# Performance work log

Measured on AMD Instinct MI355X. Metric: run time of the kernel, lower is better.

The kernel has to match this reference:

```python
import jax, jax.numpy as jnp
import numpy as np
from jax import lax

KEY_SIZE, WIDTH, CH = 4, 32, 3  # hardcoded in construct_mapping(4, 32, 3)


def _inv_perm():
    # Reproduce construct_mapping: mapping[0]=arange, mapping[1]=t (a permutation).
    # tensor_map does out[:, t[i]] = in[:, i]  ==>  out = in[:, argsort(t)].
    s = np.arange(KEY_SIZE * WIDTH * CH)
    x = s.reshape(KEY_SIZE, WIDTH, CH)
    blocks = [x[:, j:j + KEY_SIZE, :].reshape(-1) for j in range(0, WIDTH, KEY_SIZE)]
    t = np.stack(blocks, 0).reshape(-1)
    return np.argsort(t)

_INV = jnp.asarray(_inv_perm())  # [384]


def setup_inputs() -> dict:
    key = jax.random.key(0)
    ks = jax.random.split(key, 8)
    B = 8192
    return {
        "x": jax.random.normal(ks[0], (B, 32, 32, 3), jnp.float32),
        "W": jax.random.normal(ks[1], (48, 48), jnp.float32) / np.float32(np.sqrt(48.0)),
        "conv1_w": jax.random.normal(ks[2], (10, 3, 5, 5), jnp.float32) * 0.1,
        "conv1_b": jnp.zeros((10,), jnp.float32),
        "conv2_w": jax.random.normal(ks[3], (20, 10, 5, 5), jnp.float32) * 0.05,
        "conv2_b": jnp.zeros((20,), jnp.float32),
        "fc1_w": jax.random.normal(ks[4], (50, 500), jnp.float32) * 0.04,
        "fc1_b": jnp.zeros((50,), jnp.float32),
        "fc2_w": jax.random.normal(ks[5], (10, 50), jnp.float32) * 0.1,
        "fc2_b": jnp.zeros((10,), jnp.float32),
    }


def _conv(x, w, b):
    y = lax.conv_general_dilated(x, w, (1, 1), 'VALID',
                                 dimension_numbers=('NCHW', 'OIHW', 'NCHW'))
    return y + b[None, :, None, None]


def _maxpool2(x):
    return lax.reduce_window(x, -jnp.inf, lax.max, (1, 1, 2, 2), (1, 1, 2, 2), 'VALID')


def reference(x, W, conv1_w, conv1_b, conv2_w, conv2_b, fc1_w, fc1_b, fc2_w, fc2_b):
    B = x.shape[0]
    # 4x4x3 blocks in row-major block order (i outer, j inner): [B, 64, 48]
    xb = x.reshape(B, 8, 4, 8, 4, 3).transpose(0, 1, 3, 2, 4, 5).reshape(B, 64, 48)
    y = jnp.einsum('bnk,jk->bnj', xb, W)          # per-block Linear (no bias), batched GEMM
    y = y.reshape(B, 8, 384)[:, :, _INV]          # per-row permutation (fused gather)
    img = y.reshape(B, 32, 32, 3).transpose(0, 3, 1, 2)  # NHWC -> NCHW
    h = jax.nn.relu(_maxpool2(_conv(img, conv1_w, conv1_b)))       # [B,10,14,14]
    h = jax.nn.relu(_maxpool2(_conv(h, conv2_w, conv2_b)))         # dropout2d: eval = identity; [B,20,5,5]
    h = h.reshape(-1, 500)
    h = jax.nn.relu(h @ fc1_w.T + fc1_b)          # dropout: eval = identity
    logits = h @ fc2_w.T + fc2_b
    return jax.nn.log_softmax(logits, axis=-1)
```

## Files before the change

kernel.cpp:

```cpp
#include <hip/hip_runtime.h>
#include <math.h>


typedef __attribute__((ext_vector_type(8))) short bf16x8;
typedef __attribute__((ext_vector_type(4))) float f32x4;

union Frag { short4 h[2]; bf16x8 v; };

static __device__ __forceinline__ unsigned short f2bf(float f) {
    union { float f; unsigned u; } v; v.f = f;
    unsigned r = v.u + 0x7FFFu + ((v.u >> 16) & 1u);
    return (unsigned short)(r >> 16);
}

#define MFMA(a, b, c) __builtin_amdgcn_mfma_f32_16x16x32_bf16((a), (b), (c), 0, 0, 0)

__global__ __launch_bounds__(64)
void prepack(const float* __restrict__ W, const float* __restrict__ w1,
             const float* __restrict__ w2, unsigned short* __restrict__ ws) {
    const int fid = blockIdx.x;
    const int lane = threadIdx.x;
    const int col = lane & 15, grp = lane >> 4;
    unsigned short tmp[8];
    #pragma unroll
    for (int e = 0; e < 8; ++e) {
        const int kap = 16 * (e >> 2) + 4 * grp + (e & 3);
        float v = 0.f;
        if (fid < 6) {
            const int ks = fid / 3, nt = fid % 3;
            const int k = 32 * ks + kap, j = 16 * nt + col;
            if (k < 48) v = W[j * 48 + k];
        } else if (fid < 11) {
            const int ky = fid - 6;
            const int kx = kap >> 2, icp = kap & 3;
            if (kx < 5 && icp < 3 && col < 10)
                v = w1[col * 75 + icp * 25 + ky * 5 + kx];
        } else {
            const int r = fid - 11, nt = r / 10, ky = (r % 10) >> 1, s = r & 1;
            const int idx = 32 * s + kap;
            const int kx = idx / 12, icp = idx % 12, oc = 16 * nt + col;
            if (kx < 5 && icp < 10 && oc < 20)
                v = w2[oc * 250 + icp * 25 + ky * 5 + kx];
        }
        tmp[e] = f2bf(v);
    }
    Frag f;
    f.h[0] = make_short4((short)tmp[0], (short)tmp[1], (short)tmp[2], (short)tmp[3]);
    f.h[1] = make_short4((short)tmp[4], (short)tmp[5], (short)tmp[6], (short)tmp[7]);
    *(bf16x8*)(ws + fid * 512 + lane * 8) = f.v;
}

__global__ __launch_bounds__(256)
void pack_fc1(const float* __restrict__ fw1, unsigned short* __restrict__ ws) {
    const int i = blockIdx.x * 256 + threadIdx.x;
    if (i < 12500) {
        const unsigned lo = f2bf(fw1[2 * i]);
        const unsigned hi = f2bf(fw1[2 * i + 1]);
        ((unsigned*)(ws + 16384))[i] = lo | (hi << 16);
    }
}

#define RS1 160
#define IMG_SZ 5184
#define RS2 168
#define H1_SZ 2416
#define AUXF 848

__global__ __launch_bounds__(512)
void fused_net(const float* __restrict__ x,
               const unsigned short* __restrict__ ws,
               const float* __restrict__ b1,
               const float* __restrict__ b2,
               const float* __restrict__ fb1,
               const float* __restrict__ fw2,
               const float* __restrict__ fb2,
               float* __restrict__ out)
{
    const int tid  = threadIdx.x;
    const int wave = __builtin_amdgcn_readfirstlane(tid >> 6);
    const int img  = wave >> 2;
    const int wv   = wave & 3;
    const int lane = tid & 63;
    const int col16 = lane & 15, grp = lane >> 4;

    __shared__ __align__(16) unsigned short s_pool[2 * IMG_SZ];
    __shared__ __align__(16) unsigned short s_h1[2 * H1_SZ];
    __shared__ __align__(16) float s_aux[2 * AUXF];

    unsigned short* s_img = s_pool + img * IMG_SZ;
    unsigned short* s_h1i = s_h1 + img * H1_SZ;
    unsigned short* s_b2  = s_pool;
    float* aux    = s_aux + img * AUXF;
    float* s_h2   = aux;

    const size_t bb = (size_t)(2 * blockIdx.x + img);

    {
        const int blkA = 16 * wv + col16;
        const float* xb = x + bb * 3072 + (blkA >> 3) * 384 + (blkA & 7) * 12;
        const int k0 = 4 * grp,      o0 = (k0 / 12) * 96 + (k0 % 12);
        const int k1 = 16 + 4 * grp, o1 = (k1 / 12) * 96 + (k1 % 12);
        const int k2 = 32 + 4 * grp, o2 = (k2 / 12) * 96 + (k2 % 12);
        const float4 fa = *(const float4*)(xb + o0);
        const float4 fb = *(const float4*)(xb + o1);
        const float4 fc = *(const float4*)(xb + o2);
        Frag a0, a1;
        a0.h[0] = make_short4((short)f2bf(fa.x), (short)f2bf(fa.y), (short)f2bf(fa.z), (short)f2bf(fa.w));
        a0.h[1] = make_short4((short)f2bf(fb.x), (short)f2bf(fb.y), (short)f2bf(fb.z), (short)f2bf(fb.w));
        a1.h[0] = make_short4((short)f2bf(fc.x), (short)f2bf(fc.y), (short)f2bf(fc.z), (short)f2bf(fc.w));
        a1.h[1] = make_short4(0, 0, 0, 0);

        #pragma unroll
        for (int nt = 0; nt < 3; ++nt) {
            Frag bl0, bl1;
            bl0.v = *(const bf16x8*)(ws + nt * 512 + lane * 8);
            bl1.v = *(const bf16x8*)(ws + (3 + nt) * 512 + lane * 8);
            f32x4 acc = {0.f, 0.f, 0.f, 0.f};
            acc = MFMA(a0.v, bl0.v, acc);
            acc = MFMA(a1.v, bl1.v, acc);
            const int j = 16 * nt + col16;
            const int di = j / 12, dj = (j % 12) / 3, cch = j % 3;
            #pragma unroll
            for (int r = 0; r < 4; ++r) {
                const int blk = 16 * wv + 4 * grp + r;
                const int row = (blk >> 3) * 4 + di, cp = (blk & 7) * 4 + dj;
                s_img[row * RS1 + cp * 4 + cch] = f2bf(acc[r]);
            }
        }
    }
    for (int p = tid; p < 2048; p += 512) {
        unsigned short* si = s_pool + (p >> 10) * IMG_SZ;
        const int q = p & 1023;
        si[(q >> 5) * RS1 + (q & 31) * 4 + 3] = 0;
    }
    for (int p = tid; p < 2048; p += 512) {
        unsigned short* si = s_pool + (p >> 10) * IMG_SZ;
        const int q = p & 1023;
        si[(q >> 5) * RS1 + 128 + (q & 31)] = 0;
    }
    if (tid < 128) s_pool[(tid >> 6) * IMG_SZ + 32 * RS1 + (tid & 63)] = 0;
    if (tid < 128) s_h1[(tid >> 6) * H1_SZ + 14 * RS2 + (tid & 63)] = 0;
    __syncthreads();

    {
        Frag bc1[5];
        #pragma unroll
        for (int f = 0; f < 5; ++f)
            bc1[f].v = *(const bf16x8*)(ws + (6 + f) * 512 + lane * 8);
        const float bias1 = b1[col16 < 10 ? col16 : 0];

        for (int t = wv; t < 49; t += 4) {
            const int q = 4 * t + (col16 >> 2), sub = col16 & 3;
            const int oi = q / 14, oj = q % 14;
            const int ci = 2 * oi + (sub >> 1), cj = 2 * oj + (sub & 1);
            const int base = ci * RS1 + cj * 4 + 4 * grp;
            f32x4 acc = {0.f, 0.f, 0.f, 0.f};
            #pragma unroll
            for (int ky = 0; ky < 5; ++ky) {
                Frag a;
                a.h[0] = *(const short4*)&s_img[base + ky * RS1];
                a.h[1] = *(const short4*)&s_img[base + ky * RS1 + 16];
                acc = MFMA(a.v, bc1[ky].v, acc);
            }
            const int qo = 4 * t + grp;
            if (col16 < 12) {
                const float pm = fmaxf(fmaxf(acc[0], acc[1]), fmaxf(acc[2], acc[3]));
                const float val = fmaxf(pm + bias1, 0.f);
                s_h1i[(qo / 14) * RS2 + (qo % 14) * 12 + col16] =
                    (col16 < 10) ? f2bf(val) : (unsigned short)0;
            }
        }
    }
    __syncthreads();

    {
        const uint4* src = (const uint4*)(ws + 11 * 512);
        uint4* dst = (uint4*)s_pool;
        dst[tid]       = src[tid];
        dst[tid + 512] = src[tid + 512];
        if (tid < 256) dst[tid + 1024] = src[tid + 1024];
    }
    __syncthreads();

    {
        const int oc1 = 16 + col16;
        const float bias20 = b2[col16];
        const float bias21 = b2[oc1 < 20 ? oc1 : 0];

        int baseA[2];
        #pragma unroll
        for (int tt = 0; tt < 2; ++tt) {
            const int t = wv + 4 * tt;
            int q = 4 * t + (col16 >> 2); if (q > 24) q = 24;
            const int sub = col16 & 3;
            const int oi = q / 5, oj = q % 5;
            const int ci = 2 * oi + (sub >> 1), cj = 2 * oj + (sub & 1);
            baseA[tt] = ci * RS2 + cj * 12 + 4 * grp;
        }

        f32x4 accA0 = {0.f,0.f,0.f,0.f}, accA1 = {0.f,0.f,0.f,0.f};
        f32x4 accB0 = {0.f,0.f,0.f,0.f}, accB1 = {0.f,0.f,0.f,0.f};
        #pragma unroll
        for (int ky = 0; ky < 5; ++ky) {
            #pragma unroll
            for (int s = 0; s < 2; ++s) {
                Frag bb0, bb1;
                bb0.v = *(const bf16x8*)(s_b2 + (ky * 2 + s) * 512 + lane * 8);
                bb1.v = *(const bf16x8*)(s_b2 + (10 + ky * 2 + s) * 512 + lane * 8);
                Frag a0, a1;
                a0.h[0] = *(const short4*)&s_h1i[baseA[0] + ky * RS2 + 32 * s];
                a0.h[1] = *(const short4*)&s_h1i[baseA[0] + ky * RS2 + 32 * s + 16];
                a1.h[0] = *(const short4*)&s_h1i[baseA[1] + ky * RS2 + 32 * s];
                a1.h[1] = *(const short4*)&s_h1i[baseA[1] + ky * RS2 + 32 * s + 16];
                accA0 = MFMA(a0.v, bb0.v, accA0);
                accA1 = MFMA(a0.v, bb1.v, accA1);
                accB0 = MFMA(a1.v, bb0.v, accB0);
                accB1 = MFMA(a1.v, bb1.v, accB1);
            }
        }
        #pragma unroll
        for (int tt = 0; tt < 2; ++tt) {
            const int t = wv + 4 * tt;
            if (t < 7) {
                const f32x4 c0 = tt ? accB0 : accA0;
                const f32x4 c1 = tt ? accB1 : accA1;
                const int qo = 4 * t + grp;
                if (qo < 25) {
                    const float p0 = fmaxf(fmaxf(c0[0], c0[1]), fmaxf(c0[2], c0[3]));
                    s_h2[col16 * 25 + qo] = fmaxf(p0 + bias20, 0.f);
                    if (oc1 < 20) {
                        const float p1 = fmaxf(fmaxf(c1[0], c1[1]), fmaxf(c1[2], c1[3]));
                        s_h2[oc1 * 25 + qo] = fmaxf(p1 + bias21, 0.f);
                    }
                }
            }
        }
    }
    __syncthreads();

    if (tid < 500) {
        const int im = (tid >= 250) ? 1 : 0;
        const int r = tid - 250 * im;
        const int oc = r / 5, part = r % 5;
        const unsigned* wr = (const unsigned*)(ws + 16384 + oc * 500 + part * 100);
        const float* hp = s_aux + im * AUXF + part * 100;
        float a = 0.f;
        #pragma unroll
        for (int i = 0; i < 25; ++i) {
            const float4 hv = *(const float4*)(hp + 4 * i);
            const unsigned ua = wr[2 * i], ub = wr[2 * i + 1];
            a += __uint_as_float(ua << 16)          * hv.x
               + __uint_as_float(ua & 0xffff0000u) * hv.y
               + __uint_as_float(ub << 16)          * hv.z
               + __uint_as_float(ub & 0xffff0000u) * hv.w;
        }
        s_aux[im * AUXF + 512 + r] = a;
    }
    __syncthreads();
    if (tid < 100) {
        const int im = (tid >= 50) ? 1 : 0;
        const int r = tid - 50 * im;
        float a = fb1[r];
        #pragma unroll
        for (int j = 0; j < 5; ++j) a += s_aux[im * AUXF + 512 + r * 5 + j];
        s_aux[im * AUXF + 768 + r] = fmaxf(a, 0.f);
    }
    __syncthreads();

    if (tid < 20) {
        const int im = (tid >= 10) ? 1 : 0;
        const int r = tid - 10 * im;
        const float* wr = fw2 + r * 50;
        const float* f1 = s_aux + im * AUXF + 768;
        float a = fb2[r];
        for (int k = 0; k < 50; ++k) a += f1[k] * wr[k];
        s_aux[im * AUXF + 832 + r] = a;
    }
    __syncthreads();

    if (tid < 20) {
        const int im = (tid >= 10) ? 1 : 0;
        const int r = tid - 10 * im;
        const float* lg = s_aux + im * AUXF + 832;
        float m = lg[0];
        for (int k = 1; k < 10; ++k) m = fmaxf(m, lg[k]);
        float s = 0.f;
        for (int k = 0; k < 10; ++k) s += expf(lg[k] - m);
        out[(2 * (size_t)blockIdx.x + im) * 10 + r] = lg[r] - m - logf(s);
    }
}

extern "C" void kernel_launch(void* const* d_in, const int* in_sizes, int n_in,
                              void* d_out, int out_size, void* d_ws, size_t ws_size,
                              hipStream_t stream) {
    const float* x   = (const float*)d_in[0];
    const float* W   = (const float*)d_in[1];
    const float* w1  = (const float*)d_in[2];
    const float* b1  = (const float*)d_in[3];
    const float* w2  = (const float*)d_in[4];
    const float* b2  = (const float*)d_in[5];
    const float* fw1 = (const float*)d_in[6];
    const float* fb1 = (const float*)d_in[7];
    const float* fw2 = (const float*)d_in[8];
    const float* fb2 = (const float*)d_in[9];
    float* o = (float*)d_out;
    unsigned short* wsp = (unsigned short*)d_ws;

    const int B = in_sizes[0] / 3072;
    prepack<<<dim3(31), dim3(64), 0, stream>>>(W, w1, w2, wsp);
    pack_fc1<<<dim3(49), dim3(256), 0, stream>>>(fw1, wsp);
    fused_net<<<dim3(B / 2), dim3(512), 0, stream>>>(x, wsp, b1, b2, fb1, fw2, fb2, o);
}
```

Before: 110.0 us.

## Compute fc1 with bf16 MFMA using prepacked weight fragments

Rewrites fc1 from a scalar dot-product stage (500 threads, each walking 100 elements, followed by a 5-way reduction) into MFMA 16x16x32 bf16 tiles. All eight waves take part, split by output tile and K half, and a small cross-wave sum follows. fc1 weights are now prepacked into MFMA B-fragment layout, conv2 outputs are stored as bf16 with zeroed K padding, and shared memory for the aux stage shrinks. The goal is to shorten the serial tail after conv2. In exchange, the fc1 input is rounded to bf16 and most MFMA columns are wasted, since only 2 images occupy the N dimension.

```diff
diff --git a/kernel.cpp b/kernel.cpp
--- a/kernel.cpp
+++ b/kernel.cpp
@@ -50,21 +50,31 @@
     *(bf16x8*)(ws + fid * 512 + lane * 8) = f.v;
 }
 
-__global__ __launch_bounds__(256)
+__global__ __launch_bounds__(64)
 void pack_fc1(const float* __restrict__ fw1, unsigned short* __restrict__ ws) {
-    const int i = blockIdx.x * 256 + threadIdx.x;
-    if (i < 12500) {
-        const unsigned lo = f2bf(fw1[2 * i]);
-        const unsigned hi = f2bf(fw1[2 * i + 1]);
-        ((unsigned*)(ws + 16384))[i] = lo | (hi << 16);
-    }
+    const int fid = blockIdx.x;
+    const int kstep = fid >> 2, mt = fid & 3;
+    const int lane = threadIdx.x;
+    const int col = lane & 15, grp = lane >> 4;
+    const int outr = 16 * mt + col;
+    unsigned short tmp[8];
+    #pragma unroll
+    for (int e = 0; e < 8; ++e) {
+        const int kap = 16 * (e >> 2) + 4 * grp + (e & 3);
+        const int kk = 32 * kstep + kap;
+        float v = (outr < 50 && kk < 500) ? fw1[outr * 500 + kk] : 0.f;
+        tmp[e] = f2bf(v);
+    }
+    Frag f;
+    f.h[0] = make_short4((short)tmp[0], (short)tmp[1], (short)tmp[2], (short)tmp[3]);
+    f.h[1] = make_short4((short)tmp[4], (short)tmp[5], (short)tmp[6], (short)tmp[7]);
+    *(bf16x8*)(ws + 16384 + fid * 512 + lane * 8) = f.v;
 }
 
 #define RS1 160
 #define IMG_SZ 5184
 #define RS2 168
 #define H1_SZ 2416
-#define AUXF 848
 
 __global__ __launch_bounds__(512)
 void fused_net(const float* __restrict__ x,
@@ -85,13 +95,15 @@
 
     __shared__ __align__(16) unsigned short s_pool[2 * IMG_SZ];
     __shared__ __align__(16) unsigned short s_h1[2 * H1_SZ];
-    __shared__ __align__(16) float s_aux[2 * AUXF];
+    __shared__ __align__(16) unsigned short s_h2b[2 * 512];
+    __shared__ __align__(16) float s_aux[416];
 
     unsigned short* s_img = s_pool + img * IMG_SZ;
     unsigned short* s_h1i = s_h1 + img * H1_SZ;
     unsigned short* s_b2  = s_pool;
-    float* aux    = s_aux + img * AUXF;
-    float* s_h2   = aux;
+    float* s_part = s_aux;
+    float* s_f1   = s_aux + 256;
+    float* s_lg   = s_aux + 384;
 
     const size_t bb = (size_t)(2 * blockIdx.x + img);
 
@@ -140,6 +152,7 @@
     }
     if (tid < 128) s_pool[(tid >> 6) * IMG_SZ + 32 * RS1 + (tid & 63)] = 0;
     if (tid < 128) s_h1[(tid >> 6) * H1_SZ + 14 * RS2 + (tid & 63)] = 0;
+    if (tid < 24) s_h2b[(tid / 12) * 512 + 500 + (tid % 12)] = 0;
     __syncthreads();
 
     {
@@ -218,6 +231,7 @@
                 accB1 = MFMA(a1.v, bb1.v, accB1);
             }
         }
+        unsigned short* h2 = s_h2b + img * 512;
         #pragma unroll
         for (int tt = 0; tt < 2; ++tt) {
             const int t = wv + 4 * tt;
@@ -227,10 +241,10 @@
                 const int qo = 4 * t + grp;
                 if (qo < 25) {
                     const float p0 = fmaxf(fmaxf(c0[0], c0[1]), fmaxf(c0[2], c0[3]));
-                    s_h2[col16 * 25 + qo] = fmaxf(p0 + bias20, 0.f);
+                    h2[col16 * 25 + qo] = f2bf(fmaxf(p0 + bias20, 0.f));
                     if (oc1 < 20) {
                         const float p1 = fmaxf(fmaxf(c1[0], c1[1]), fmaxf(c1[2], c1[3]));
-                        s_h2[oc1 * 25 + qo] = fmaxf(p1 + bias21, 0.f);
+                        h2[oc1 * 25 + qo] = f2bf(fmaxf(p1 + bias21, 0.f));
                     }
                 }
             }
@@ -238,32 +252,30 @@
     }
     __syncthreads();
 
-    if (tid < 500) {
-        const int im = (tid >= 250) ? 1 : 0;
-        const int r = tid - 250 * im;
-        const int oc = r / 5, part = r % 5;
-        const unsigned* wr = (const unsigned*)(ws + 16384 + oc * 500 + part * 100);
-        const float* hp = s_aux + im * AUXF + part * 100;
-        float a = 0.f;
-        #pragma unroll
-        for (int i = 0; i < 25; ++i) {
-            const float4 hv = *(const float4*)(hp + 4 * i);
-            const unsigned ua = wr[2 * i], ub = wr[2 * i + 1];
-            a += __uint_as_float(ua << 16)          * hv.x
-               + __uint_as_float(ua & 0xffff0000u) * hv.y
-               + __uint_as_float(ub << 16)          * hv.z
-               + __uint_as_float(ub & 0xffff0000u) * hv.w;
-        }
-        s_aux[im * AUXF + 512 + r] = a;
-    }
-    __syncthreads();
-    if (tid < 100) {
-        const int im = (tid >= 50) ? 1 : 0;
-        const int r = tid - 50 * im;
-        float a = fb1[r];
-        #pragma unroll
-        for (int j = 0; j < 5; ++j) a += s_aux[im * AUXF + 512 + r * 5 + j];
-        s_aux[im * AUXF + 768 + r] = fmaxf(a, 0.f);
+    {
+        const int mt = wv, khalf = img;
+        const int imc = col16 < 2 ? col16 : 0;
+        f32x4 acc = {0.f, 0.f, 0.f, 0.f};
+        #pragma unroll
+        for (int j = 0; j < 8; ++j) {
+            const int kstep = 8 * khalf + j;
+            Frag af, bfv;
+            af.v = *(const bf16x8*)(ws + 16384 + (kstep * 4 + mt) * 512 + lane * 8);
+            bfv.h[0] = *(const short4*)&s_h2b[imc * 512 + 32 * kstep + 4 * grp];
+            bfv.h[1] = *(const short4*)&s_h2b[imc * 512 + 32 * kstep + 16 + 4 * grp];
+            acc = MFMA(af.v, bfv.v, acc);
+        }
+        if (col16 < 2) {
+            #pragma unroll
+            for (int r = 0; r < 4; ++r)
+                s_part[(khalf * 2 + col16) * 64 + 16 * mt + 4 * grp + r] = acc[r];
+        }
+    }
+    __syncthreads();
+    if (tid < 128) {
+        const int im = tid >> 6, o = tid & 63;
+        const float a = s_part[im * 64 + o] + s_part[(2 + im) * 64 + o];
+        if (o < 50) s_f1[im * 64 + o] = fmaxf(a + fb1[o], 0.f);
     }
     __syncthreads();
 
@@ -271,17 +283,17 @@
         const int im = (tid >= 10) ? 1 : 0;
         const int r = tid - 10 * im;
         const float* wr = fw2 + r * 50;
-        const float* f1 = s_aux + im * AUXF + 768;
+        const float* f1 = s_f1 + im * 64;
         float a = fb2[r];
         for (int k = 0; k < 50; ++k) a += f1[k] * wr[k];
-        s_aux[im * AUXF + 832 + r] = a;
+        s_lg[im * 16 + r] = a;
     }
     __syncthreads();
 
     if (tid < 20) {
         const int im = (tid >= 10) ? 1 : 0;
         const int r = tid - 10 * im;
-        const float* lg = s_aux + im * AUXF + 832;
+        const float* lg = s_lg + im * 16;
         float m = lg[0];
         for (int k = 1; k < 10; ++k) m = fmaxf(m, lg[k]);
         float s = 0.f;
@@ -308,6 +320,6 @@
 
     const int B = in_sizes[0] / 3072;
     prepack<<<dim3(31), dim3(64), 0, stream>>>(W, w1, w2, wsp);
-    pack_fc1<<<dim3(49), dim3(256), 0, stream>>>(fw1, wsp);
+    pack_fc1<<<dim3(64), dim3(64), 0, stream>>>(fw1, wsp);
     fused_net<<<dim3(B / 2), dim3(512), 0, stream>>>(x, wsp, b1, b2, fb1, fw2, fb2, o);
 }
```

After: 89.15 us. -18.9%, faster.
